# Kernel tuning notes

Hardware: AMD Instinct MI355X
Metric: run time of the kernel (lower is better)

Reference implementation:

```python
import jax, jax.numpy as jnp
import numpy as np

B, H, S, D = 4, 8, 2048, 64
NEG = -1e9


def setup_inputs() -> dict:
    key = jax.random.key(0)
    k1, k2, k3, k4 = jax.random.split(key, 4)
    qs = jax.random.normal(k1, (B, H, S, D), dtype=jnp.float32)
    ks = jax.random.normal(k2, (B, H, S, D), dtype=jnp.float32)
    vs = jax.random.normal(k3, (B, H, S, D), dtype=jnp.float32)
    # binary 0/1 float mask, broadcast over heads
    mask = (jax.random.uniform(k4, (B, 1, S, S)) < 0.5).astype(jnp.float32)
    return {"qs": qs, "ks": ks, "vs": vs, "mask": mask}


def reference(qs, ks, vs, mask):
    scale = 1.0 / np.sqrt(qs.shape[-1]).astype(np.float32)
    # [B,H,S,S] logits; multiplicative pre-mask, then additive -1e9 on masked slots
    logits = jnp.einsum('bhqd,bhkd->bhqk', qs, ks) * mask * scale
    logits = logits + (1.0 - mask) * NEG
    weights = jax.nn.softmax(logits, axis=-1) * mask  # multiplicative post-mask
    return jnp.einsum('bhqk,bhkd->bhqd', weights, vs)
```

## Files before the change

kernel.cpp:

```cpp
#include <hip/hip_runtime.h>
#include <stdint.h>

#define S_LEN 2048
#define NTILE 32

typedef float f32x4 __attribute__((ext_vector_type(4)));
typedef short bf16x8 __attribute__((ext_vector_type(8)));
typedef uint32_t u32x2 __attribute__((ext_vector_type(2)));

__device__ __forceinline__ uint16_t f2bf(float f) {
    uint32_t u = __float_as_uint(f);
    return (uint16_t)((u + 0x7FFFu + ((u >> 16) & 1u)) >> 16);
}

#define SWZ(r, cb) (((r) << 7) + ((cb) ^ (((r) & 7) << 4)))

#define AS3PTR(p) ((__attribute__((address_space(3))) uint32_t*)(uintptr_t)(p))
#define AS1PTR(p) ((const __attribute__((address_space(1))) uint32_t*)(uintptr_t)(p))

__global__ __launch_bounds__(256) void prep_k(const float* __restrict__ K,
                                              uint8_t* __restrict__ Kswz) {
    int flat = blockIdx.x * 256 + threadIdx.x;
    int cb = flat & 7, r = (flat >> 3) & 63, kt = (flat >> 9) & 31, bh = flat >> 14;
    const float* src = K + (((size_t)bh * S_LEN + kt * 64 + r) << 6) + cb * 8;
    f32x4 a = *(const f32x4*)src;
    f32x4 b = *(const f32x4*)(src + 4);
    bf16x8 o;
    o[0] = (short)f2bf(a[0]); o[1] = (short)f2bf(a[1]);
    o[2] = (short)f2bf(a[2]); o[3] = (short)f2bf(a[3]);
    o[4] = (short)f2bf(b[0]); o[5] = (short)f2bf(b[1]);
    o[6] = (short)f2bf(b[2]); o[7] = (short)f2bf(b[3]);
    *(bf16x8*)(Kswz + (((size_t)(bh * 32 + kt)) << 13) + SWZ(r, cb * 16)) = o;
}

__global__ __launch_bounds__(256) void prep_v(const float* __restrict__ V,
                                              uint8_t* __restrict__ Vtswz) {
    int flat = blockIdx.x * 256 + threadIdx.x;
    int d = flat & 63, ck = (flat >> 6) & 7, kt = (flat >> 9) & 31, bh = flat >> 14;
    const float* src = V + (((size_t)bh * S_LEN + kt * 64 + ck * 8) << 6) + d;
    bf16x8 o;
    #pragma unroll
    for (int i = 0; i < 8; ++i) o[i] = (short)f2bf(src[i << 6]);
    *(bf16x8*)(Vtswz + (((size_t)(bh * 32 + kt)) << 13) + SWZ(d, ck * 16)) = o;
}

__global__ __launch_bounds__(256) void prep_m(const float* __restrict__ M,
                                              unsigned long long* __restrict__ Mb) {
    int wave = blockIdx.x * 4 + (threadIdx.x >> 6);
    int lane = threadIdx.x & 63;
    size_t w0 = (size_t)wave * 64;
    for (int i = 0; i < 64; ++i) {
        size_t widx = w0 + i;
        float m = M[(widx << 6) + lane];
        unsigned long long bits = __ballot(m > 0.5f);
        if (lane == 0) Mb[widx] = bits;
    }
}

#define K_OFF 0
#define V_OFF 16384
#define P_OFF 32768

__global__ __launch_bounds__(256, 4)
void attn_fwd(const float* __restrict__ Q, const uint8_t* __restrict__ Kswz,
              const uint8_t* __restrict__ Vtswz,
              const unsigned long long* __restrict__ Mb,
              float* __restrict__ O)
{
    __shared__ __align__(16) uint8_t lds[40960];

    const int tid  = threadIdx.x;
    const int lane = tid & 63;
    const int w    = tid >> 6;
    const int g    = lane >> 4;
    const int c    = lane & 15;

    const int bid = blockIdx.x;
    const int bh  = bid >> 5;
    const int qt  = bid & 31;
    const int b   = bh >> 3;
    const int q0  = qt << 6;

    bf16x8 qf[2];
    {
        const float* qrow = Q + (((size_t)bh * S_LEN + q0 + w * 16 + c) << 6);
        #pragma unroll
        for (int kb = 0; kb < 2; ++kb) {
            f32x4 a  = *(const f32x4*)(qrow + kb * 32 + g * 8);
            f32x4 b4 = *(const f32x4*)(qrow + kb * 32 + g * 8 + 4);
            bf16x8 f;
            f[0] = (short)f2bf(a[0]);  f[1] = (short)f2bf(a[1]);
            f[2] = (short)f2bf(a[2]);  f[3] = (short)f2bf(a[3]);
            f[4] = (short)f2bf(b4[0]); f[5] = (short)f2bf(b4[1]);
            f[6] = (short)f2bf(b4[2]); f[7] = (short)f2bf(b4[3]);
            qf[kb] = f;
        }
    }

    f32x4 acc[4];
    #pragma unroll
    for (int dt = 0; dt < 4; ++dt) acc[dt] = (f32x4){0.f, 0.f, 0.f, 0.f};
    float lsum = 0.f;

    const float SCL2 = 0.125f * 1.44269504088896340736f;

    const unsigned long long* mrow =
        Mb + ((size_t)(b * S_LEN + q0 + w * 16 + c) << 5);

    const uint8_t* kbh = Kswz  + ((size_t)(bh * 32) << 13);
    const uint8_t* vbh = Vtswz + ((size_t)(bh * 32) << 13);

    auto stage = [&](int buf, int t) {
        #pragma unroll
        for (int it = 0; it < 2; ++it) {
            int off = ((w << 1) + it) << 10;
            __builtin_amdgcn_global_load_lds(
                AS1PTR(kbh + ((size_t)t << 13) + off + lane * 16),
                AS3PTR(&lds[K_OFF + (buf << 13) + off]), 16, 0, 0);
            __builtin_amdgcn_global_load_lds(
                AS1PTR(vbh + ((size_t)t << 13) + off + lane * 16),
                AS3PTR(&lds[V_OFF + (buf << 13) + off]), 16, 0, 0);
        }
    };

    stage(0, 0);
    __syncthreads();

    #pragma unroll 2
    for (int kt = 0; kt < NTILE; ++kt) {
        const int buf = kt & 1;
        if (kt + 1 < NTILE) stage(buf ^ 1, kt + 1);

        unsigned long long mw = mrow[kt];

        const uint8_t* kb = &lds[K_OFF + (buf << 13)];
        f32x4 sacc[4];
        #pragma unroll
        for (int ct = 0; ct < 4; ++ct) {
            bf16x8 kf0 = *(const bf16x8*)(kb + SWZ(16 * ct + c, 16 * g));
            bf16x8 kf1 = *(const bf16x8*)(kb + SWZ(16 * ct + c, 64 + 16 * g));
            f32x4 z = (f32x4){0.f, 0.f, 0.f, 0.f};
            z = __builtin_amdgcn_mfma_f32_16x16x32_bf16(kf0, qf[0], z, 0, 0, 0);
            z = __builtin_amdgcn_mfma_f32_16x16x32_bf16(kf1, qf[1], z, 0, 0, 0);
            sacc[ct] = z;
        }

        unsigned long long msh = mw >> (4 * g);
        uint32_t ulo = (uint32_t)msh;
        uint32_t uhi = (uint32_t)(msh >> 32);
        #pragma unroll
        for (int ct = 0; ct < 4; ++ct) {
            uint32_t sel = (ct & 2) ? uhi : ulo;
            float e[4];
            #pragma unroll
            for (int j = 0; j < 4; ++j) {
                float x = sacc[ct][j] * SCL2;
                x = (sel & (1u << (16 * (ct & 1) + j))) ? x : -1000.f;
                asm("v_exp_f32 %0, %1" : "=v"(e[j]) : "v"(x));
                lsum += e[j];
            }
            uint32_t lo, hi;
            asm("v_cvt_pk_bf16_f32 %0, %1, %2" : "=v"(lo) : "v"(e[0]), "v"(e[1]));
            asm("v_cvt_pk_bf16_f32 %0, %1, %2" : "=v"(hi) : "v"(e[2]), "v"(e[3]));
            u32x2 pw = {lo, hi};
            *(u32x2*)(&lds[P_OFF + (w << 11) + SWZ(c, 32 * ct + 8 * g)]) = pw;
        }

        const uint8_t* vb = &lds[V_OFF + (buf << 13)];
        #pragma unroll
        for (int kp = 0; kp < 2; ++kp) {
            bf16x8 pf = *(const bf16x8*)(&lds[P_OFF + (w << 11) +
                                              SWZ(c, kp * 64 + 16 * g)]);
            #pragma unroll
            for (int dt = 0; dt < 4; ++dt) {
                bf16x8 vf = *(const bf16x8*)(vb + SWZ(c + 16 * dt, kp * 64 + 16 * g));
                acc[dt] = __builtin_amdgcn_mfma_f32_16x16x32_bf16(pf, vf, acc[dt], 0, 0, 0);
            }
        }

        __syncthreads();
    }

    float l = lsum;
    l += __shfl_xor(l, 16, 64);
    l += __shfl_xor(l, 32, 64);
    float linv = (l > 0.f) ? 1.f / l : 0.f;
    float inv[4];
    #pragma unroll
    for (int j = 0; j < 4; ++j) inv[j] = __shfl(linv, 4 * g + j, 64);

    float* obase = O + (((size_t)bh * S_LEN + q0 + w * 16) << 6);
    #pragma unroll
    for (int j = 0; j < 4; ++j)
        #pragma unroll
        for (int dt = 0; dt < 4; ++dt)
            obase[((4 * g + j) << 6) + c + 16 * dt] = acc[dt][j] * inv[j];
}

extern "C" void kernel_launch(void* const* d_in, const int* in_sizes, int n_in,
                              void* d_out, int out_size, void* d_ws, size_t ws_size,
                              hipStream_t stream) {
    const float* qs   = (const float*)d_in[0];
    const float* ks   = (const float*)d_in[1];
    const float* vs   = (const float*)d_in[2];
    const float* mask = (const float*)d_in[3];
    float* out = (float*)d_out;
    (void)in_sizes; (void)n_in; (void)out_size; (void)ws_size;

    uint8_t* ws = (uint8_t*)d_ws;
    uint8_t* Kswz  = ws;
    uint8_t* Vtswz = ws + (8u << 20);
    unsigned long long* Mb = (unsigned long long*)(ws + (16u << 20));

    hipLaunchKernelGGL(prep_k, dim3(2048), dim3(256), 0, stream, ks, Kswz);
    hipLaunchKernelGGL(prep_v, dim3(2048), dim3(256), 0, stream, vs, Vtswz);
    hipLaunchKernelGGL(prep_m, dim3(1024), dim3(256), 0, stream, mask, Mb);
    hipLaunchKernelGGL(attn_fwd, dim3(1024), dim3(256), 0, stream,
                       qs, Kswz, Vtswz, Mb, out);
}
```

Measured before the change: 96.87 us.

## Fuse prep kernels, keep P in registers via permlane swaps, fold scale into Q

Merges the three preprocessing kernels into one launch and spreads the mask packing over more blocks. In the attention kernel, the softmax probabilities are rearranged in registers with permlane32/16 swaps instead of a round trip through LDS, which frees 8KB of shared memory. The score scale is folded into Q before the bf16 conversion, and blocks are remapped so that consecutive block IDs cover different heads. This removes launch overhead, LDS traffic and one multiply per score, but rounds the pre-scaled Q to bf16 differently from before and depends on the permlane lane mapping being correct.

```diff
diff --git a/kernel.cpp b/kernel.cpp
--- a/kernel.cpp
+++ b/kernel.cpp
@@ -6,7 +6,6 @@
 
 typedef float f32x4 __attribute__((ext_vector_type(4)));
 typedef short bf16x8 __attribute__((ext_vector_type(8)));
-typedef uint32_t u32x2 __attribute__((ext_vector_type(2)));
 
 __device__ __forceinline__ uint16_t f2bf(float f) {
     uint32_t u = __float_as_uint(f);
@@ -18,48 +17,48 @@
 #define AS3PTR(p) ((__attribute__((address_space(3))) uint32_t*)(uintptr_t)(p))
 #define AS1PTR(p) ((const __attribute__((address_space(1))) uint32_t*)(uintptr_t)(p))
 
-__global__ __launch_bounds__(256) void prep_k(const float* __restrict__ K,
-                                              uint8_t* __restrict__ Kswz) {
-    int flat = blockIdx.x * 256 + threadIdx.x;
-    int cb = flat & 7, r = (flat >> 3) & 63, kt = (flat >> 9) & 31, bh = flat >> 14;
-    const float* src = K + (((size_t)bh * S_LEN + kt * 64 + r) << 6) + cb * 8;
-    f32x4 a = *(const f32x4*)src;
-    f32x4 b = *(const f32x4*)(src + 4);
-    bf16x8 o;
-    o[0] = (short)f2bf(a[0]); o[1] = (short)f2bf(a[1]);
-    o[2] = (short)f2bf(a[2]); o[3] = (short)f2bf(a[3]);
-    o[4] = (short)f2bf(b[0]); o[5] = (short)f2bf(b[1]);
-    o[6] = (short)f2bf(b[2]); o[7] = (short)f2bf(b[3]);
-    *(bf16x8*)(Kswz + (((size_t)(bh * 32 + kt)) << 13) + SWZ(r, cb * 16)) = o;
-}
-
-__global__ __launch_bounds__(256) void prep_v(const float* __restrict__ V,
-                                              uint8_t* __restrict__ Vtswz) {
-    int flat = blockIdx.x * 256 + threadIdx.x;
-    int d = flat & 63, ck = (flat >> 6) & 7, kt = (flat >> 9) & 31, bh = flat >> 14;
-    const float* src = V + (((size_t)bh * S_LEN + kt * 64 + ck * 8) << 6) + d;
-    bf16x8 o;
-    #pragma unroll
-    for (int i = 0; i < 8; ++i) o[i] = (short)f2bf(src[i << 6]);
-    *(bf16x8*)(Vtswz + (((size_t)(bh * 32 + kt)) << 13) + SWZ(d, ck * 16)) = o;
-}
-
-__global__ __launch_bounds__(256) void prep_m(const float* __restrict__ M,
-                                              unsigned long long* __restrict__ Mb) {
-    int wave = blockIdx.x * 4 + (threadIdx.x >> 6);
-    int lane = threadIdx.x & 63;
-    size_t w0 = (size_t)wave * 64;
-    for (int i = 0; i < 64; ++i) {
-        size_t widx = w0 + i;
-        float m = M[(widx << 6) + lane];
-        unsigned long long bits = __ballot(m > 0.5f);
-        if (lane == 0) Mb[widx] = bits;
+__global__ __launch_bounds__(256)
+void prep_all(const float* __restrict__ K, const float* __restrict__ V,
+              const float* __restrict__ M, uint8_t* __restrict__ Kswz,
+              uint8_t* __restrict__ Vtswz, unsigned long long* __restrict__ Mb)
+{
+    const int bid = blockIdx.x;
+    const int tid = threadIdx.x;
+    if (bid < 2048) {
+        int flat = bid * 256 + tid;
+        int cb = flat & 7, r = (flat >> 3) & 63, kt = (flat >> 9) & 31, bh = flat >> 14;
+        const float* src = K + (((size_t)bh * S_LEN + kt * 64 + r) << 6) + cb * 8;
+        f32x4 a = *(const f32x4*)src;
+        f32x4 b = *(const f32x4*)(src + 4);
+        bf16x8 o;
+        o[0] = (short)f2bf(a[0]); o[1] = (short)f2bf(a[1]);
+        o[2] = (short)f2bf(a[2]); o[3] = (short)f2bf(a[3]);
+        o[4] = (short)f2bf(b[0]); o[5] = (short)f2bf(b[1]);
+        o[6] = (short)f2bf(b[2]); o[7] = (short)f2bf(b[3]);
+        *(bf16x8*)(Kswz + (((size_t)(bh * 32 + kt)) << 13) + SWZ(r, cb * 16)) = o;
+    } else if (bid < 4096) {
+        int flat = (bid - 2048) * 256 + tid;
+        int d = flat & 63, ck = (flat >> 6) & 7, kt = (flat >> 9) & 31, bh = flat >> 14;
+        const float* src = V + (((size_t)bh * S_LEN + kt * 64 + ck * 8) << 6) + d;
+        bf16x8 o;
+        #pragma unroll
+        for (int i = 0; i < 8; ++i) o[i] = (short)f2bf(src[i << 6]);
+        *(bf16x8*)(Vtswz + (((size_t)(bh * 32 + kt)) << 13) + SWZ(d, ck * 16)) = o;
+    } else {
+        int wave = (bid - 4096) * 4 + (tid >> 6);
+        int lane = tid & 63;
+        size_t w0 = (size_t)wave * 16;
+        for (int i = 0; i < 16; ++i) {
+            size_t widx = w0 + i;
+            float m = M[(widx << 6) + lane];
+            unsigned long long bits = __ballot(m > 0.5f);
+            if (lane == 0) Mb[widx] = bits;
+        }
     }
 }
 
 #define K_OFF 0
 #define V_OFF 16384
-#define P_OFF 32768
 
 __global__ __launch_bounds__(256, 4)
 void attn_fwd(const float* __restrict__ Q, const uint8_t* __restrict__ Kswz,
@@ -67,7 +66,7 @@
               const unsigned long long* __restrict__ Mb,
               float* __restrict__ O)
 {
-    __shared__ __align__(16) uint8_t lds[40960];
+    __shared__ __align__(16) uint8_t lds[32768];
 
     const int tid  = threadIdx.x;
     const int lane = tid & 63;
@@ -75,12 +74,14 @@
     const int g    = lane >> 4;
     const int c    = lane & 15;
 
-    const int bid = blockIdx.x;
+    const int bid0 = blockIdx.x;
+    const int bid  = ((bid0 & 7) << 7) + (bid0 >> 3);
     const int bh  = bid >> 5;
     const int qt  = bid & 31;
     const int b   = bh >> 3;
     const int q0  = qt << 6;
 
+    const float QSCL = 0.125f * 1.44269504088896340736f;
     bf16x8 qf[2];
     {
         const float* qrow = Q + (((size_t)bh * S_LEN + q0 + w * 16 + c) << 6);
@@ -89,10 +90,10 @@
             f32x4 a  = *(const f32x4*)(qrow + kb * 32 + g * 8);
             f32x4 b4 = *(const f32x4*)(qrow + kb * 32 + g * 8 + 4);
             bf16x8 f;
-            f[0] = (short)f2bf(a[0]);  f[1] = (short)f2bf(a[1]);
-            f[2] = (short)f2bf(a[2]);  f[3] = (short)f2bf(a[3]);
-            f[4] = (short)f2bf(b4[0]); f[5] = (short)f2bf(b4[1]);
-            f[6] = (short)f2bf(b4[2]); f[7] = (short)f2bf(b4[3]);
+            f[0] = (short)f2bf(a[0] * QSCL);  f[1] = (short)f2bf(a[1] * QSCL);
+            f[2] = (short)f2bf(a[2] * QSCL);  f[3] = (short)f2bf(a[3] * QSCL);
+            f[4] = (short)f2bf(b4[0] * QSCL); f[5] = (short)f2bf(b4[1] * QSCL);
+            f[6] = (short)f2bf(b4[2] * QSCL); f[7] = (short)f2bf(b4[3] * QSCL);
             qf[kb] = f;
         }
     }
@@ -101,8 +102,6 @@
     #pragma unroll
     for (int dt = 0; dt < 4; ++dt) acc[dt] = (f32x4){0.f, 0.f, 0.f, 0.f};
     float lsum = 0.f;
-
-    const float SCL2 = 0.125f * 1.44269504088896340736f;
 
     const unsigned long long* mrow =
         Mb + ((size_t)(b * S_LEN + q0 + w * 16 + c) << 5);
@@ -145,36 +144,39 @@
             sacc[ct] = z;
         }
 
+        uint32_t pd[4][2];
         unsigned long long msh = mw >> (4 * g);
-        uint32_t ulo = (uint32_t)msh;
-        uint32_t uhi = (uint32_t)(msh >> 32);
+        uint32_t ulo = (uint32_t)msh, uhi = (uint32_t)(msh >> 32);
         #pragma unroll
         for (int ct = 0; ct < 4; ++ct) {
             uint32_t sel = (ct & 2) ? uhi : ulo;
             float e[4];
             #pragma unroll
             for (int j = 0; j < 4; ++j) {
-                float x = sacc[ct][j] * SCL2;
+                float x = sacc[ct][j];
                 x = (sel & (1u << (16 * (ct & 1) + j))) ? x : -1000.f;
                 asm("v_exp_f32 %0, %1" : "=v"(e[j]) : "v"(x));
                 lsum += e[j];
             }
-            uint32_t lo, hi;
-            asm("v_cvt_pk_bf16_f32 %0, %1, %2" : "=v"(lo) : "v"(e[0]), "v"(e[1]));
-            asm("v_cvt_pk_bf16_f32 %0, %1, %2" : "=v"(hi) : "v"(e[2]), "v"(e[3]));
-            u32x2 pw = {lo, hi};
-            *(u32x2*)(&lds[P_OFF + (w << 11) + SWZ(c, 32 * ct + 8 * g)]) = pw;
+            asm("v_cvt_pk_bf16_f32 %0, %1, %2" : "=v"(pd[ct][0]) : "v"(e[0]), "v"(e[1]));
+            asm("v_cvt_pk_bf16_f32 %0, %1, %2" : "=v"(pd[ct][1]) : "v"(e[2]), "v"(e[3]));
         }
 
         const uint8_t* vb = &lds[V_OFF + (buf << 13)];
         #pragma unroll
         for (int kp = 0; kp < 2; ++kp) {
-            bf16x8 pf = *(const bf16x8*)(&lds[P_OFF + (w << 11) +
-                                              SWZ(c, kp * 64 + 16 * g)]);
+            uint32_t a0 = pd[2 * kp][0], b0 = pd[2 * kp + 1][0];
+            uint32_t a1 = pd[2 * kp][1], b1 = pd[2 * kp + 1][1];
+            asm("v_permlane32_swap_b32 %0, %1" : "+v"(a0), "+v"(b0));
+            asm("v_permlane16_swap_b32 %0, %1" : "+v"(a0), "+v"(b0));
+            asm("v_permlane32_swap_b32 %0, %1" : "+v"(a1), "+v"(b1));
+            asm("v_permlane16_swap_b32 %0, %1" : "+v"(a1), "+v"(b1));
+            union { uint32_t d[4]; bf16x8 v; } pu;
+            pu.d[0] = a0; pu.d[1] = a1; pu.d[2] = b0; pu.d[3] = b1;
             #pragma unroll
             for (int dt = 0; dt < 4; ++dt) {
                 bf16x8 vf = *(const bf16x8*)(vb + SWZ(c + 16 * dt, kp * 64 + 16 * g));
-                acc[dt] = __builtin_amdgcn_mfma_f32_16x16x32_bf16(pf, vf, acc[dt], 0, 0, 0);
+                acc[dt] = __builtin_amdgcn_mfma_f32_16x16x32_bf16(pu.v, vf, acc[dt], 0, 0, 0);
             }
         }
 
@@ -212,9 +214,8 @@
     uint8_t* Vtswz = ws + (8u << 20);
     unsigned long long* Mb = (unsigned long long*)(ws + (16u << 20));
 
-    hipLaunchKernelGGL(prep_k, dim3(2048), dim3(256), 0, stream, ks, Kswz);
-    hipLaunchKernelGGL(prep_v, dim3(2048), dim3(256), 0, stream, vs, Vtswz);
-    hipLaunchKernelGGL(prep_m, dim3(1024), dim3(256), 0, stream, mask, Mb);
+    hipLaunchKernelGGL(prep_all, dim3(8192), dim3(256), 0, stream,
+                       ks, vs, mask, Kswz, Vtswz, Mb);
     hipLaunchKernelGGL(attn_fwd, dim3(1024), dim3(256), 0, stream,
                        qs, Kswz, Vtswz, Mb, out);
 }
```

After: 81.33 us. -16.0%, faster.
